# Performance work log

Measured on AMD Instinct MI355X. Metric: run time of the kernel, lower is better.

Reference implementation:

```python
import jax, jax.numpy as jnp
import numpy as np

N_NODES = 160_000
N_EDGES = 640_000
N_GRAPHS = 8_000
IN_FEATS = 74
HID = 63
MAX_DEG = 10
PRED_HID = 128
PRED_DIM = 256
BN_EPS = 1e-5
N_LAYERS = 3
PARAM_NAMES = ['W0', 'b0', 'gamma0', 'beta0', 'W1', 'b1', 'gamma1', 'beta1', 'W2', 'b2', 'gamma2', 'beta2', 'W_ng', 'b_ng', 'W_tr', 'b_tr']


def setup_inputs() -> dict:
    key = jax.random.key(0)
    ks = jax.random.split(key, 20)
    inp = {}
    inp['feats'] = jax.random.normal(ks[0], (N_NODES, IN_FEATS), dtype=jnp.float32)
    inp['src'] = jax.random.randint(ks[1], (N_EDGES,), 0, N_NODES, dtype=jnp.int32)
    inp['dst'] = jax.random.randint(ks[2], (N_EDGES,), 0, N_NODES, dtype=jnp.int32)
    # sorted graph membership: 20 nodes per graph (batched molecular graphs)
    inp['graph_ids'] = jnp.repeat(jnp.arange(N_GRAPHS, dtype=jnp.int32), N_NODES // N_GRAPHS)
    dims = [IN_FEATS, HID, HID, HID]
    for l in range(N_LAYERS):
        fi, fo = dims[l], dims[l + 1]
        inp[f'W{l}'] = jax.random.normal(ks[3 + l], (MAX_DEG, fi, fo), dtype=jnp.float32) / np.float32(np.sqrt(fi))
        inp[f'b{l}'] = jnp.zeros((MAX_DEG, fo), dtype=jnp.float32)
        inp[f'gamma{l}'] = jnp.ones((fo,), dtype=jnp.float32)
        inp[f'beta{l}'] = jnp.zeros((fo,), dtype=jnp.float32)
    inp['W_ng'] = jax.random.normal(ks[10], (HID, PRED_HID), dtype=jnp.float32) / np.float32(np.sqrt(HID))
    inp['b_ng'] = jnp.zeros((PRED_HID,), dtype=jnp.float32)
    inp['W_tr'] = jax.random.normal(ks[11], (2 * PRED_HID, PRED_DIM), dtype=jnp.float32) / np.float32(np.sqrt(2 * PRED_HID))
    inp['b_tr'] = jnp.zeros((PRED_DIM,), dtype=jnp.float32)
    return inp


def _nf_layer(h, src, dst, deg_idx, W, b, gamma, beta):
    # message passing: sum of neighbor features via copy_u / fn.sum
    neigh = jax.ops.segment_sum(h[src], dst, num_segments=N_NODES)
    tot = h + neigh  # self + neighbor sum (Duvenaud neural fingerprint)
    # degree-bucketed linear: compute all MAX_DEG transforms, select per node by degree
    z_all = jnp.einsum('ni,kio->nko', tot, W) + b  # [N, MAX_DEG, out]
    z = jnp.take_along_axis(z_all, deg_idx[:, None, None], axis=1)[:, 0, :]  # [N, out]
    z = jax.nn.relu(z)
    # batchnorm over nodes (training-mode batch statistics, eps=1e-5)
    mu = jnp.mean(z, axis=0)
    var = jnp.var(z, axis=0)
    return (z - mu) * jax.lax.rsqrt(var + BN_EPS) * gamma + beta


def _forward(feats, src, dst, graph_ids, params):
    # in-degree per node, clamped to [1, MAX_DEG] -> weight bucket index
    deg = jax.ops.segment_sum(jnp.ones((N_EDGES,), jnp.float32), dst, num_segments=N_NODES)
    deg_idx = jnp.clip(deg.astype(jnp.int32), 1, MAX_DEG) - 1
    h = feats
    for l in range(N_LAYERS):
        h = _nf_layer(h, src, dst, deg_idx, params[f'W{l}'], params[f'b{l}'],
                      params[f'gamma{l}'], params[f'beta{l}'])
    # node_to_graph linear
    h = h @ params['W_ng'] + params['b_ng']  # [N, PRED_HID]
    # SumAndMax readout over each graph
    g_sum = jax.ops.segment_sum(h, graph_ids, num_segments=N_GRAPHS)
    g_max = jax.ops.segment_max(h, graph_ids, num_segments=N_GRAPHS)
    g = jnp.tanh(jnp.concatenate([g_sum, g_max], axis=-1))  # [G, 2*PRED_HID]
    return g @ params['W_tr'] + params['b_tr']  # [G, PRED_DIM]


def reference(feats, src, dst, graph_ids, W0, b0, gamma0, beta0, W1, b1, gamma1, beta1, W2, b2, gamma2, beta2, W_ng, b_ng, W_tr, b_tr):
    params = dict(zip(PARAM_NAMES, (W0, b0, gamma0, beta0, W1, b1, gamma1, beta1, W2, b2, gamma2, beta2, W_ng, b_ng, W_tr, b_tr)))
    return _forward(feats, src, dst, graph_ids, params)
```

## Files before the change

kernel.cpp:

```cpp
#include <hip/hip_runtime.h>
#include <stdint.h>
#include <math.h>

static constexpr int NN = 160000;
static constexpr int NE = 640000;
static constexpr int NG = 8000;
static constexpr int FH  = 63;
static constexpr int ZST = 64;
static constexpr int FST = 80;
static constexpr int NB  = 128;
static constexpr int LGRID = 1536;

static constexpr size_t OFF_DEGCNT = 0;
static constexpr size_t OFF_CURSOR = 640000;
static constexpr size_t OFF_BCNT   = 1280000;
static constexpr size_t OFF_SPART  = 1280064;
static constexpr size_t ZERO_BYTES = 1673280;
static constexpr size_t OFF_ROWPTR = 1673280;
static constexpr size_t OFF_BLKSUM = 2313472;
static constexpr size_t OFF_COL    = 2315520;
static constexpr size_t OFF_BLIST  = 4875520;
static constexpr size_t OFF_AFC    = 17675520;
static constexpr size_t OFF_BNG2   = 17709312;
static constexpr size_t OFF_PBLK   = 17709824;
static constexpr size_t OFF_FB     = 17710080;
static constexpr size_t OFF_Z0     = 43310080;
static constexpr size_t OFF_Z1     = 63790080;
static constexpr size_t OFF_WNGF   = OFF_Z1;
static constexpr size_t OFF_WTRF   = OFF_Z1 + 32768;

__device__ __forceinline__ float blo(unsigned u) {
    union { unsigned i; float f; } v; v.i = u << 16; return v.f;
}
__device__ __forceinline__ float bhi(unsigned u) {
    union { unsigned i; float f; } v; v.i = u & 0xffff0000u; return v.f;
}
__device__ __forceinline__ unsigned short f2b(float f) {
    union { float f; unsigned i; } v; v.f = f;
    unsigned r = v.i + 0x7fffu + ((v.i >> 16) & 1u);
    return (unsigned short)(r >> 16);
}
__device__ __forceinline__ void acc8(float* a, uint4 q) {
    a[0] += blo(q.x); a[1] += bhi(q.x);
    a[2] += blo(q.y); a[3] += bhi(q.y);
    a[4] += blo(q.z); a[5] += bhi(q.z);
    a[6] += blo(q.w); a[7] += bhi(q.w);
}

typedef __attribute__((ext_vector_type(8))) short bf16x8;
typedef __attribute__((ext_vector_type(4))) float f32x4;
union U8 { uint4 u; bf16x8 b; };

__global__ void k_cast(const float* __restrict__ feats, unsigned short* __restrict__ fb,
                       const int* __restrict__ dst, int* __restrict__ degcnt) {
    int i = blockIdx.x * 256 + threadIdx.x;
    if (i < NE) atomicAdd(&degcnt[dst[i]], 1);
    if (i >= NN * FST) return;
    int n = i / FST, c = i - n * FST;
    float v = (c < 74) ? feats[n * 74 + c] : 0.f;
    union { float f; unsigned u; } x; x.f = v;
    unsigned r = x.u + 0x7fffu + ((x.u >> 16) & 1u);
    fb[i] = (unsigned short)(r >> 16);
}

__global__ void k_scan1(const int* __restrict__ degcnt, int* __restrict__ row_ptr,
                        int* __restrict__ blksum) {
    __shared__ int s[1024];
    int t = threadIdx.x;
    int i = blockIdx.x * 1024 + t;
    int v = (i < NN) ? degcnt[i] : 0;
    s[t] = v; __syncthreads();
    for (int off = 1; off < 1024; off <<= 1) {
        int x = (t >= off) ? s[t - off] : 0;
        __syncthreads();
        s[t] += x;
        __syncthreads();
    }
    if (i < NN) row_ptr[i + 1] = s[t];
    if (t == 1023) blksum[blockIdx.x] = s[t];
}

__global__ void k_scan2(int* __restrict__ blksum, int nblk) {
    __shared__ int s[256];
    int t = threadIdx.x;
    int v = (t < nblk) ? blksum[t] : 0;
    s[t] = v; __syncthreads();
    for (int off = 1; off < 256; off <<= 1) {
        int x = (t >= off) ? s[t - off] : 0;
        __syncthreads();
        s[t] += x;
        __syncthreads();
    }
    if (t < nblk) blksum[t] = s[t] - v;
}

__global__ void k_scan3(int* __restrict__ row_ptr, const int* __restrict__ blksum) {
    int t = threadIdx.x;
    int i = blockIdx.x * 1024 + t;
    if (i < NN) row_ptr[i + 1] += blksum[blockIdx.x];
    if (i == 0) row_ptr[0] = 0;
}

__global__ void __launch_bounds__(1024) k_bucket(
        const int* __restrict__ degcnt, const int* __restrict__ row_ptr,
        int* __restrict__ bcnt, int2* __restrict__ blist,
        int* __restrict__ pblk, int* __restrict__ ctr) {
    __shared__ int scnt[10], sbase[10];
    __shared__ int sLast;
    int tid = threadIdx.x;
    if (tid < 10) scnt[tid] = 0;
    __syncthreads();
    int n = blockIdx.x * 1024 + tid;
    int k = 0, pos = 0;
    bool v = (n < NN);
    int rp = 0;
    if (v) {
        int d = degcnt[n];
        rp = row_ptr[n];
        k = (d < 1) ? 0 : ((d > 10) ? 9 : d - 1);
        pos = atomicAdd(&scnt[k], 1);
    }
    __syncthreads();
    if (tid < 10) sbase[tid] = scnt[tid] ? atomicAdd(&bcnt[tid], scnt[tid]) : 0;
    __syncthreads();
    if (v) blist[k * NN + sbase[k] + pos] = make_int2(n, rp);

    if (tid == 0) {
        __threadfence();
        sLast = (atomicAdd(ctr, 1) == (int)gridDim.x - 1) ? 1 : 0;
    }
    __syncthreads();
    if (sLast && tid == 0) {
        __threadfence();
        const volatile int* bc = bcnt;
        int s = 0; pblk[0] = 0;
        for (int kk = 0; kk < 10; ++kk) { s += (bc[kk] + NB - 1) / NB; pblk[kk + 1] = s; }
    }
}

__global__ void k_fill(const int* __restrict__ src, const int* __restrict__ dst,
                       const int* __restrict__ row_ptr, int* __restrict__ cursor,
                       int* __restrict__ col) {
    int e = blockIdx.x * 256 + threadIdx.x;
    if (e >= NE) return;
    int d = dst[e];
    int pos = row_ptr[d] + atomicAdd(&cursor[d], 1);
    col[pos] = src[e];
}

template<int FI, int IST, bool AFF>
__global__ void __launch_bounds__(512, 4) k_layer(
    const unsigned short* __restrict__ in,
    const float* __restrict__ aff,
    const int* __restrict__ row_ptr, const int* __restrict__ col,
    const int* __restrict__ bcnt, const int2* __restrict__ blist,
    const int* __restrict__ pblk,
    const float* __restrict__ W, const float* __restrict__ B,
    unsigned short* __restrict__ zout, float* __restrict__ spart)
{
    constexpr int CH = IST / 8;
    __shared__ float sW[FI * 63 + 64];
    __shared__ float sTot[8][IST][8];
    __shared__ int   sN[8][8];
    __shared__ float sRed[2][8][64];

    int b = blockIdx.x;
    if (b >= pblk[10]) return;
    int k = 0;
#pragma unroll
    for (int i = 1; i <= 9; ++i) k += (b >= pblk[i]) ? 1 : 0;
    int base = (b - pblk[k]) * NB;
    int cnt = bcnt[k];
    if (base >= cnt) return;

    int tid = threadIdx.x;
    int wave = tid >> 6, lane = tid & 63;
    int t = lane >> 3, r = lane & 7;

    const float* Wk = W + (size_t)k * FI * 63;
#pragma unroll 4
    for (int i = tid; i < FI * 63; i += 512) sW[i] = Wk[i];
    __syncthreads();

    const uint4* inq = (const uint4*)in;
    float bterm = (lane < 63) ? B[k * 63 + lane] : 0.f;
    float lsum = 0.f, lsq = 0.f;

#pragma unroll 1
    for (int it = 0; it < NB / 64; ++it) {
        int idx = base + it * 64 + wave * 8 + t;
        if (base + it * 64 >= cnt) break;
        bool val = (idx < cnt);
        int2 bl = blist[k * NN + (val ? idx : (cnt - 1))];
        int n = bl.x, rs = bl.y;
        int dg = (k >= 1 && k <= 8) ? (k + 1) : (row_ptr[n + 1] - rs);
        if (r == 0) sN[wave][t] = val ? n : -1;

        float a[8] = {0.f, 0.f, 0.f, 0.f, 0.f, 0.f, 0.f, 0.f};

        if (k == 9) {
            {
                uint4 q = inq[(size_t)n * CH + r];
                acc8(a, q);
            }
            int d = 0;
#pragma unroll 1
            for (; d + 4 <= dg; d += 4) {
                int c0 = col[rs + d], c1 = col[rs + d + 1];
                int c2 = col[rs + d + 2], c3 = col[rs + d + 3];
                uint4 q0 = inq[(size_t)c0 * CH + r];
                uint4 q1 = inq[(size_t)c1 * CH + r];
                uint4 q2 = inq[(size_t)c2 * CH + r];
                uint4 q3 = inq[(size_t)c3 * CH + r];
                acc8(a, q0); acc8(a, q1); acc8(a, q2); acc8(a, q3);
            }
#pragma unroll 1
            for (; d < dg; ++d) {
                int c = col[rs + d];
                uint4 q = inq[(size_t)c * CH + r];
                acc8(a, q);
            }
            if constexpr (IST == 80) {
                float e2[8] = {0.f, 0.f, 0.f, 0.f, 0.f, 0.f, 0.f, 0.f};
                if (r < 2) {
                    uint4 q = inq[(size_t)n * CH + 8 + r];
                    acc8(e2, q);
                    int d2 = 0;
#pragma unroll 1
                    for (; d2 < dg; ++d2) {
                        int c = col[rs + d2];
                        uint4 p = inq[(size_t)c * CH + 8 + r];
                        acc8(e2, p);
                    }
#pragma unroll
                    for (int j = 0; j < 8; ++j) sTot[wave][64 + 8 * r + j][t] = e2[j];
                }
            }
        } else {
            if constexpr (IST == 80) {
                if (r < 2) {
                    float e2[8] = {0.f, 0.f, 0.f, 0.f, 0.f, 0.f, 0.f, 0.f};
                    uint4 ps = inq[(size_t)n * CH + 8 + r];
                    uint4 p0, p1, p2, p3, p4, p5, p6, p7, p8;
                    if (dg > 0) p0 = inq[(size_t)col[rs + 0] * CH + 8 + r];
                    if (dg > 1) p1 = inq[(size_t)col[rs + 1] * CH + 8 + r];
                    if (dg > 2) p2 = inq[(size_t)col[rs + 2] * CH + 8 + r];
                    if (dg > 3) p3 = inq[(size_t)col[rs + 3] * CH + 8 + r];
                    if (dg > 4) p4 = inq[(size_t)col[rs + 4] * CH + 8 + r];
                    if (dg > 5) p5 = inq[(size_t)col[rs + 5] * CH + 8 + r];
                    if (dg > 6) p6 = inq[(size_t)col[rs + 6] * CH + 8 + r];
                    if (dg > 7) p7 = inq[(size_t)col[rs + 7] * CH + 8 + r];
                    if (dg > 8) p8 = inq[(size_t)col[rs + 8] * CH + 8 + r];
                    acc8(e2, ps);
                    if (dg > 0) acc8(e2, p0);
                    if (dg > 1) acc8(e2, p1);
                    if (dg > 2) acc8(e2, p2);
                    if (dg > 3) acc8(e2, p3);
                    if (dg > 4) acc8(e2, p4);
                    if (dg > 5) acc8(e2, p5);
                    if (dg > 6) acc8(e2, p6);
                    if (dg > 7) acc8(e2, p7);
                    if (dg > 8) acc8(e2, p8);
#pragma unroll
                    for (int j = 0; j < 8; ++j) sTot[wave][64 + 8 * r + j][t] = e2[j];
                }
            }
            uint4 qs = inq[(size_t)n * CH + r];
            uint4 q0, q1, q2, q3, q4, q5, q6, q7, q8;
            if (dg > 0) q0 = inq[(size_t)col[rs + 0] * CH + r];
            if (dg > 1) q1 = inq[(size_t)col[rs + 1] * CH + r];
            if (dg > 2) q2 = inq[(size_t)col[rs + 2] * CH + r];
            if (dg > 3) q3 = inq[(size_t)col[rs + 3] * CH + r];
            if (dg > 4) q4 = inq[(size_t)col[rs + 4] * CH + r];
            if (dg > 5) q5 = inq[(size_t)col[rs + 5] * CH + r];
            if (dg > 6) q6 = inq[(size_t)col[rs + 6] * CH + r];
            if (dg > 7) q7 = inq[(size_t)col[rs + 7] * CH + r];
            if (dg > 8) q8 = inq[(size_t)col[rs + 8] * CH + r];
            acc8(a, qs);
            if (dg > 0) acc8(a, q0);
            if (dg > 1) acc8(a, q1);
            if (dg > 2) acc8(a, q2);
            if (dg > 3) acc8(a, q3);
            if (dg > 4) acc8(a, q4);
            if (dg > 5) acc8(a, q5);
            if (dg > 6) acc8(a, q6);
            if (dg > 7) acc8(a, q7);
            if (dg > 8) acc8(a, q8);
        }

        if constexpr (AFF) {
            const float4* af = (const float4*)aff;
            float4 A0 = af[2 * r], A1 = af[2 * r + 1];
            float4 C0 = af[16 + 2 * r], C1 = af[16 + 2 * r + 1];
            float dp1 = (float)(dg + 1);
            a[0] = A0.x * a[0] + dp1 * C0.x;  a[1] = A0.y * a[1] + dp1 * C0.y;
            a[2] = A0.z * a[2] + dp1 * C0.z;  a[3] = A0.w * a[3] + dp1 * C0.w;
            a[4] = A1.x * a[4] + dp1 * C1.x;  a[5] = A1.y * a[5] + dp1 * C1.y;
            a[6] = A1.z * a[6] + dp1 * C1.z;  a[7] = A1.w * a[7] + dp1 * C1.w;
        }

#pragma unroll
        for (int j = 0; j < 8; ++j) sTot[wave][8 * r + j][t] = a[j];

        float acc[8];
#pragma unroll
        for (int i = 0; i < 8; ++i) acc[i] = bterm;
#pragma unroll 4
        for (int j = 0; j < FI; ++j) {
            float w = sW[j * 63 + lane];
            float4 u = *(const float4*)&sTot[wave][j][0];
            float4 v = *(const float4*)&sTot[wave][j][4];
            acc[0] = fmaf(u.x, w, acc[0]); acc[1] = fmaf(u.y, w, acc[1]);
            acc[2] = fmaf(u.z, w, acc[2]); acc[3] = fmaf(u.w, w, acc[3]);
            acc[4] = fmaf(v.x, w, acc[4]); acc[5] = fmaf(v.y, w, acc[5]);
            acc[6] = fmaf(v.z, w, acc[6]); acc[7] = fmaf(v.w, w, acc[7]);
        }

#pragma unroll
        for (int tt = 0; tt < 8; ++tt) {
            int nn = sN[wave][tt];
            float z = fmaxf(acc[tt], 0.f);
            if (nn >= 0 && lane < 63) {
                zout[(size_t)nn * ZST + lane] = f2b(z);
                lsum += z; lsq += z * z;
            }
        }
    }

    sRed[0][wave][lane] = lsum;
    sRed[1][wave][lane] = lsq;
    __syncthreads();
    if (wave == 0 && lane < 63) {
        float s = 0.f, q = 0.f;
#pragma unroll
        for (int w8 = 0; w8 < 8; ++w8) {
            s += sRed[0][w8][lane];
            q += sRed[1][w8][lane];
        }
        float* sp = spart + (size_t)(blockIdx.x & 255) * 128;
        atomicAdd(&sp[lane], s);
        atomicAdd(&sp[64 + lane], q);
    }
}

__global__ void k_bn(const float* __restrict__ spart, const float* __restrict__ gamma,
                     const float* __restrict__ beta, float* __restrict__ afc) {
    __shared__ double sd[512];
    int o = blockIdx.x;
    int t = threadIdx.x;
    sd[t]       = (double)spart[t * 128 + o];
    sd[256 + t] = (double)spart[t * 128 + 64 + o];
    __syncthreads();
#pragma unroll
    for (int off = 128; off > 0; off >>= 1) {
        if (t < off) { sd[t] += sd[t + off]; sd[256 + t] += sd[256 + t + off]; }
        __syncthreads();
    }
    if (t == 0) {
        double mu  = sd[0] / NN;
        double var = sd[256] / NN - mu * mu;
        float a = (float)((double)gamma[o] / sqrt(var + 1e-5));
        float c = (float)((double)beta[o] - mu * (double)a);
        afc[o] = a;
        afc[64 + o] = c;
    }
}

__global__ void k_prepw(const float* __restrict__ W_ng, const float* __restrict__ b_ng,
                        const float* __restrict__ afc2, const float* __restrict__ W_tr,
                        unsigned short* __restrict__ WngF, unsigned short* __restrict__ WtrF,
                        float* __restrict__ bng2) {
    int bid = blockIdx.x, tid = threadIdx.x;
    if (bid == 0) {
        if (tid < 128) {
            float acc = b_ng[tid];
            for (int j = 0; j < 63; ++j)
                acc = fmaf(afc2[64 + j], W_ng[j * 128 + tid], acc);
            bng2[tid] = acc;
        }
    } else if (bid <= 64) {
        int idx = (bid - 1) * 256 + tid;
        int j = idx & 7, lane = (idx >> 3) & 63;
        int nt = (idx >> 9) & 7, kb = idx >> 12;
        int k = (kb & 1) * 32 + ((lane >> 4) << 3) + j;
        int col = nt * 16 + (lane & 15);
        float w = (k < 63) ? afc2[k] * W_ng[k * 128 + col] : 0.f;
        unsigned short hi = f2b(w);
        if (kb < 2) WngF[idx] = hi;
        else        WngF[idx] = f2b(w - blo(hi));
    } else {
        int idx = (bid - 65) * 256 + tid;
        int j = idx & 7, lane = (idx >> 3) & 63;
        int kb = (idx >> 9) & 7, nt = idx >> 12;
        int k = kb * 32 + ((lane >> 4) << 3) + j;
        int col = nt * 16 + (lane & 15);
        WtrF[idx] = f2b(W_tr[k * 256 + col]);
    }
}

__global__ void __launch_bounds__(256, 2) k_graph(
    const unsigned short* __restrict__ Z2, const unsigned short* __restrict__ WngF,
    const float* __restrict__ bng2, const unsigned short* __restrict__ WtrF,
    const float* __restrict__ b_tr, float* __restrict__ out)
{
    __shared__ unsigned short sW[16384];
    __shared__ float sT[16 * 256];
    __shared__ float sB[128];

    int tid = threadIdx.x;
    int wave = tid >> 6, lane = tid & 63;
    int gl15 = lane & 15, grp = lane >> 4;

    {
        const uint4* srcq = (const uint4*)WngF;
        uint4* dstq = (uint4*)sW;
#pragma unroll
        for (int i = 0; i < 8; ++i) dstq[tid + 256 * i] = srcq[tid + 256 * i];
    }
    if (tid < 128) sB[tid] = bng2[tid];
    __syncthreads();

    int nodeBase = blockIdx.x * 320 + wave * 80;
    const uint4* zq = (const uint4*)Z2;
    uint4 a0[5], a1[5];
#pragma unroll
    for (int m = 0; m < 5; ++m) {
        size_t row = (size_t)(nodeBase + m * 16 + gl15) * 8;
        a0[m] = zq[row + grp];
        a1[m] = zq[row + 4 + grp];
    }
    if (grp == 3) {
#pragma unroll
        for (int m = 0; m < 5; ++m) a1[m].w &= 0xffffu;
    }

    const uint4* swq = (const uint4*)sW;
    const float NEGI = -3.0e38f;

#pragma unroll 1
    for (int nt = 0; nt < 8; ++nt) {
        U8 b0, b1, b2, b3;
        b0.u = swq[(0 * 8 + nt) * 64 + lane];
        b1.u = swq[(1 * 8 + nt) * 64 + lane];
        b2.u = swq[(2 * 8 + nt) * 64 + lane];
        b3.u = swq[(3 * 8 + nt) * 64 + lane];

        f32x4 ac[5];
#pragma unroll
        for (int m = 0; m < 5; ++m) {
            U8 xa0, xa1; xa0.u = a0[m]; xa1.u = a1[m];
            f32x4 c = {0.f, 0.f, 0.f, 0.f};
            c = __builtin_amdgcn_mfma_f32_16x16x32_bf16(xa0.b, b0.b, c, 0, 0, 0);
            c = __builtin_amdgcn_mfma_f32_16x16x32_bf16(xa1.b, b1.b, c, 0, 0, 0);
            c = __builtin_amdgcn_mfma_f32_16x16x32_bf16(xa0.b, b2.b, c, 0, 0, 0);
            c = __builtin_amdgcn_mfma_f32_16x16x32_bf16(xa1.b, b3.b, c, 0, 0, 0);
            ac[m] = c;
        }

        float s[4] = {0.f, 0.f, 0.f, 0.f};
        float x[4] = {NEGI, NEGI, NEGI, NEGI};
        bool cA = lane < 16, cB = lane < 32, cC = lane < 48;
#pragma unroll
        for (int r = 0; r < 4; ++r) {
            float v0 = ac[0][r]; s[0] += v0; x[0] = fmaxf(x[0], v0);
            float v4 = ac[4][r]; s[3] += v4; x[3] = fmaxf(x[3], v4);
            float v1 = ac[1][r]; float v1a = cA ? v1 : 0.f;
            s[0] += v1a; s[1] += v1 - v1a;
            x[0] = fmaxf(x[0], cA ? v1 : NEGI); x[1] = fmaxf(x[1], cA ? NEGI : v1);
            float v2 = ac[2][r]; float v2a = cB ? v2 : 0.f;
            s[1] += v2a; s[2] += v2 - v2a;
            x[1] = fmaxf(x[1], cB ? v2 : NEGI); x[2] = fmaxf(x[2], cB ? NEGI : v2);
            float v3 = ac[3][r]; float v3a = cC ? v3 : 0.f;
            s[2] += v3a; s[3] += v3 - v3a;
            x[2] = fmaxf(x[2], cC ? v3 : NEGI); x[3] = fmaxf(x[3], cC ? NEGI : v3);
        }
#pragma unroll
        for (int g = 0; g < 4; ++g) {
            s[g] += __shfl_xor(s[g], 16);
            s[g] += __shfl_xor(s[g], 32);
            x[g] = fmaxf(x[g], __shfl_xor(x[g], 16));
            x[g] = fmaxf(x[g], __shfl_xor(x[g], 32));
        }
        if (lane < 16) {
            int c = nt * 16 + lane;
            float bb = sB[c];
#pragma unroll
            for (int g = 0; g < 4; ++g) {
                int row = wave * 4 + g;
                int swz = (row & 7) << 2;
                sT[(row * 256 + c) ^ swz]       = tanhf(s[g] + 20.f * bb);
                sT[(row * 256 + 128 + c) ^ swz] = tanhf(x[g] + bb);
            }
        }
    }
    __syncthreads();

    U8 pa[8];
    {
        int swz = (gl15 & 7) << 2;
#pragma unroll
        for (int kb = 0; kb < 8; ++kb) {
            int k8 = kb * 32 + grp * 8;
            float4 t0 = *(const float4*)&sT[(gl15 * 256 + k8) ^ swz];
            float4 t1 = *(const float4*)&sT[(gl15 * 256 + k8 + 4) ^ swz];
            unsigned u0 = (unsigned)f2b(t0.x) | ((unsigned)f2b(t0.y) << 16);
            unsigned u1 = (unsigned)f2b(t0.z) | ((unsigned)f2b(t0.w) << 16);
            unsigned u2 = (unsigned)f2b(t1.x) | ((unsigned)f2b(t1.y) << 16);
            unsigned u3 = (unsigned)f2b(t1.z) | ((unsigned)f2b(t1.w) << 16);
            pa[kb].u = make_uint4(u0, u1, u2, u3);
        }
    }
    const uint4* wtq = (const uint4*)WtrF;
    size_t gbase = (size_t)blockIdx.x * 16 * 256;
#pragma unroll 2
    for (int i = 0; i < 4; ++i) {
        int nt = wave * 4 + i;
        f32x4 c = {0.f, 0.f, 0.f, 0.f};
#pragma unroll
        for (int kb = 0; kb < 8; ++kb) {
            U8 b; b.u = wtq[(nt * 8 + kb) * 64 + lane];
            c = __builtin_amdgcn_mfma_f32_16x16x32_bf16(pa[kb].b, b.b, c, 0, 0, 0);
        }
        int d = nt * 16 + gl15;
        float btv = b_tr[d];
#pragma unroll
        for (int r = 0; r < 4; ++r) {
            int row = grp * 4 + r;
            out[gbase + (size_t)row * 256 + d] = c[r] + btv;
        }
    }
}

extern "C" void kernel_launch(void* const* d_in, const int* in_sizes, int n_in,
                              void* d_out, int out_size, void* d_ws, size_t ws_size,
                              hipStream_t stream) {
    const float* feats = (const float*)d_in[0];
    const int*   src   = (const int*)d_in[1];
    const int*   dst   = (const int*)d_in[2];
    const float* W0 = (const float*)d_in[4];
    const float* b0 = (const float*)d_in[5];
    const float* g0 = (const float*)d_in[6];
    const float* be0 = (const float*)d_in[7];
    const float* W1 = (const float*)d_in[8];
    const float* b1 = (const float*)d_in[9];
    const float* g1 = (const float*)d_in[10];
    const float* be1 = (const float*)d_in[11];
    const float* W2 = (const float*)d_in[12];
    const float* b2 = (const float*)d_in[13];
    const float* g2 = (const float*)d_in[14];
    const float* be2 = (const float*)d_in[15];
    const float* Wng = (const float*)d_in[16];
    const float* bng = (const float*)d_in[17];
    const float* Wtr = (const float*)d_in[18];
    const float* btr = (const float*)d_in[19];
    float* out = (float*)d_out;

    char* ws = (char*)d_ws;
    int*    degcnt  = (int*)(ws + OFF_DEGCNT);
    int*    cursor  = (int*)(ws + OFF_CURSOR);
    int*    bcnt    = (int*)(ws + OFF_BCNT);
    int*    ctr     = bcnt + 10;
    float*  spart   = (float*)(ws + OFF_SPART);
    int*    row_ptr = (int*)(ws + OFF_ROWPTR);
    int*    blksum  = (int*)(ws + OFF_BLKSUM);
    int*    col     = (int*)(ws + OFF_COL);
    int2*   blist   = (int2*)(ws + OFF_BLIST);
    float*  afc     = (float*)(ws + OFF_AFC);
    float*  bng2    = (float*)(ws + OFF_BNG2);
    int*    pblk    = (int*)(ws + OFF_PBLK);
    unsigned short* Fb = (unsigned short*)(ws + OFF_FB);
    unsigned short* Z0 = (unsigned short*)(ws + OFF_Z0);
    unsigned short* Z1 = (unsigned short*)(ws + OFF_Z1);
    unsigned short* Z2 = Z0;
    unsigned short* WngF = (unsigned short*)(ws + OFF_WNGF);
    unsigned short* WtrF = (unsigned short*)(ws + OFF_WTRF);

    hipMemsetAsync(d_ws, 0, ZERO_BYTES, stream);

    k_cast<<<NN * FST / 256, 256, 0, stream>>>(feats, Fb, dst, degcnt);
    k_scan1<<<157, 1024, 0, stream>>>(degcnt, row_ptr, blksum);
    k_scan2<<<1, 256, 0, stream>>>(blksum, 157);
    k_scan3<<<157, 1024, 0, stream>>>(row_ptr, blksum);
    k_bucket<<<157, 1024, 0, stream>>>(degcnt, row_ptr, bcnt, blist, pblk, ctr);
    k_fill<<<NE / 256, 256, 0, stream>>>(src, dst, row_ptr, cursor, col);

    k_layer<74, FST, false><<<LGRID, 512, 0, stream>>>(
        Fb, nullptr, row_ptr, col, bcnt, blist, pblk, W0, b0, Z0, spart);
    k_bn<<<63, 256, 0, stream>>>(spart, g0, be0, afc);
    k_layer<63, ZST, true><<<LGRID, 512, 0, stream>>>(
        Z0, afc, row_ptr, col, bcnt, blist, pblk, W1, b1, Z1, spart + 256 * 128);
    k_bn<<<63, 256, 0, stream>>>(spart + 256 * 128, g1, be1, afc + 128);
    k_layer<63, ZST, true><<<LGRID, 512, 0, stream>>>(
        Z1, afc + 128, row_ptr, col, bcnt, blist, pblk, W2, b2, Z2, spart + 2 * 256 * 128);
    k_bn<<<63, 256, 0, stream>>>(spart + 2 * 256 * 128, g2, be2, afc + 256);

    k_prepw<<<321, 256, 0, stream>>>(Wng, bng, afc + 256, Wtr, WngF, WtrF, bng2);
    k_graph<<<NG / 16, 256, 0, stream>>>(Z2, WngF, bng2, WtrF, btr, out);
}
```

Before: 500.4 us.

## Store padded per-bucket neighbor lists for aligned vector index loads

Adds a zero-initialized 12-wide neighbor table, ordered by degree-bucket slot and filled during CSR construction, for nodes with degree up to 9. The layer kernel reads all neighbor indices with three int4 loads instead of dependent scalar col[] reads. It also issues the feature gathers unconditionally so they can all be in flight together. This costs a larger zeroed workspace (about 7.7 MB more memset), extra scattered writes in k_fill, and wasted gathers of node 0 for padded slots.

```diff
diff --git a/kernel.cpp b/kernel.cpp
--- a/kernel.cpp
+++ b/kernel.cpp
@@ -15,17 +15,19 @@
 static constexpr size_t OFF_CURSOR = 640000;
 static constexpr size_t OFF_BCNT   = 1280000;
 static constexpr size_t OFF_SPART  = 1280064;
-static constexpr size_t ZERO_BYTES = 1673280;
-static constexpr size_t OFF_ROWPTR = 1673280;
-static constexpr size_t OFF_BLKSUM = 2313472;
-static constexpr size_t OFF_COL    = 2315520;
-static constexpr size_t OFF_BLIST  = 4875520;
-static constexpr size_t OFF_AFC    = 17675520;
-static constexpr size_t OFF_BNG2   = 17709312;
-static constexpr size_t OFF_PBLK   = 17709824;
-static constexpr size_t OFF_FB     = 17710080;
-static constexpr size_t OFF_Z0     = 43310080;
-static constexpr size_t OFF_Z1     = 63790080;
+static constexpr size_t OFF_NBR    = 1673280;
+static constexpr size_t ZERO_BYTES = 9353280;
+static constexpr size_t OFF_ROWPTR = 9353280;
+static constexpr size_t OFF_BLKSUM = 9994048;
+static constexpr size_t OFF_COL    = 9996096;
+static constexpr size_t OFF_NSLOT  = 12556096;
+static constexpr size_t OFF_BLIST  = 13196096;
+static constexpr size_t OFF_AFC    = 19596096;
+static constexpr size_t OFF_BNG2   = 19596864;
+static constexpr size_t OFF_PBLK   = 19597376;
+static constexpr size_t OFF_FB     = 19597504;
+static constexpr size_t OFF_Z0     = 45197504;
+static constexpr size_t OFF_Z1     = 65677504;
 static constexpr size_t OFF_WNGF   = OFF_Z1;
 static constexpr size_t OFF_WTRF   = OFF_Z1 + 32768;
 
@@ -103,7 +105,8 @@
 
 __global__ void __launch_bounds__(1024) k_bucket(
         const int* __restrict__ degcnt, const int* __restrict__ row_ptr,
-        int* __restrict__ bcnt, int2* __restrict__ blist,
+        int* __restrict__ bcnt, int* __restrict__ blist,
+        int* __restrict__ nodeslot,
         int* __restrict__ pblk, int* __restrict__ ctr) {
     __shared__ int scnt[10], sbase[10];
     __shared__ int sLast;
@@ -113,17 +116,19 @@
     int n = blockIdx.x * 1024 + tid;
     int k = 0, pos = 0;
     bool v = (n < NN);
-    int rp = 0;
     if (v) {
         int d = degcnt[n];
-        rp = row_ptr[n];
         k = (d < 1) ? 0 : ((d > 10) ? 9 : d - 1);
         pos = atomicAdd(&scnt[k], 1);
     }
     __syncthreads();
     if (tid < 10) sbase[tid] = scnt[tid] ? atomicAdd(&bcnt[tid], scnt[tid]) : 0;
     __syncthreads();
-    if (v) blist[k * NN + sbase[k] + pos] = make_int2(n, rp);
+    if (v) {
+        int slot = sbase[k] + pos;
+        blist[k * NN + slot] = n;
+        nodeslot[n] = (k << 24) | slot;
+    }
 
     if (tid == 0) {
         __threadfence();
@@ -134,18 +139,30 @@
         __threadfence();
         const volatile int* bc = bcnt;
         int s = 0; pblk[0] = 0;
-        for (int kk = 0; kk < 10; ++kk) { s += (bc[kk] + NB - 1) / NB; pblk[kk + 1] = s; }
+        int eacc = 0;
+        for (int kk = 0; kk < 10; ++kk) {
+            s += (bc[kk] + NB - 1) / NB; pblk[kk + 1] = s;
+            pblk[11 + kk] = eacc; eacc += bc[kk];
+        }
     }
 }
 
 __global__ void k_fill(const int* __restrict__ src, const int* __restrict__ dst,
                        const int* __restrict__ row_ptr, int* __restrict__ cursor,
-                       int* __restrict__ col) {
+                       int* __restrict__ col, const int* __restrict__ nodeslot,
+                       const int* __restrict__ ebase, int* __restrict__ nbr) {
     int e = blockIdx.x * 256 + threadIdx.x;
     if (e >= NE) return;
     int d = dst[e];
-    int pos = row_ptr[d] + atomicAdd(&cursor[d], 1);
-    col[pos] = src[e];
+    int sv = src[e];
+    int cur = atomicAdd(&cursor[d], 1);
+    col[row_ptr[d] + cur] = sv;
+    int s = nodeslot[d];
+    int kk = s >> 24;
+    if (kk < 9) {
+        int row = ebase[kk] + (s & 0xFFFFFF);
+        nbr[row * 12 + cur] = sv;
+    }
 }
 
 template<int FI, int IST, bool AFF>
@@ -153,8 +170,8 @@
     const unsigned short* __restrict__ in,
     const float* __restrict__ aff,
     const int* __restrict__ row_ptr, const int* __restrict__ col,
-    const int* __restrict__ bcnt, const int2* __restrict__ blist,
-    const int* __restrict__ pblk,
+    const int* __restrict__ bcnt, const int* __restrict__ blist,
+    const int* __restrict__ pblk, const int* __restrict__ nbr,
     const float* __restrict__ W, const float* __restrict__ B,
     unsigned short* __restrict__ zout, float* __restrict__ spart)
 {
@@ -172,6 +189,7 @@
     int base = (b - pblk[k]) * NB;
     int cnt = bcnt[k];
     if (base >= cnt) return;
+    int ebs = pblk[11 + k];
 
     int tid = threadIdx.x;
     int wave = tid >> 6, lane = tid & 63;
@@ -191,14 +209,17 @@
         int idx = base + it * 64 + wave * 8 + t;
         if (base + it * 64 >= cnt) break;
         bool val = (idx < cnt);
-        int2 bl = blist[k * NN + (val ? idx : (cnt - 1))];
-        int n = bl.x, rs = bl.y;
-        int dg = (k >= 1 && k <= 8) ? (k + 1) : (row_ptr[n + 1] - rs);
+        int idxc = val ? idx : (cnt - 1);
+        int n = blist[k * NN + idxc];
+        int dg;
+        if (k >= 1 && k <= 8) dg = k + 1;
+        else dg = row_ptr[n + 1] - row_ptr[n];
         if (r == 0) sN[wave][t] = val ? n : -1;
 
         float a[8] = {0.f, 0.f, 0.f, 0.f, 0.f, 0.f, 0.f, 0.f};
 
         if (k == 9) {
+            int rs = row_ptr[n];
             {
                 uint4 q = inq[(size_t)n * CH + r];
                 acc8(a, q);
@@ -237,20 +258,25 @@
                 }
             }
         } else {
+            const int4* nb4 = (const int4*)(nbr + (size_t)(ebs + idxc) * 12);
+            int4 w0 = nb4[0], w1 = nb4[1], w2 = nb4[2];
+            int c0 = w0.x, c1 = w0.y, c2 = w0.z, c3 = w0.w;
+            int c4 = w1.x, c5 = w1.y, c6 = w1.z, c7 = w1.w;
+            int c8 = w2.x;
+
             if constexpr (IST == 80) {
                 if (r < 2) {
                     float e2[8] = {0.f, 0.f, 0.f, 0.f, 0.f, 0.f, 0.f, 0.f};
                     uint4 ps = inq[(size_t)n * CH + 8 + r];
-                    uint4 p0, p1, p2, p3, p4, p5, p6, p7, p8;
-                    if (dg > 0) p0 = inq[(size_t)col[rs + 0] * CH + 8 + r];
-                    if (dg > 1) p1 = inq[(size_t)col[rs + 1] * CH + 8 + r];
-                    if (dg > 2) p2 = inq[(size_t)col[rs + 2] * CH + 8 + r];
-                    if (dg > 3) p3 = inq[(size_t)col[rs + 3] * CH + 8 + r];
-                    if (dg > 4) p4 = inq[(size_t)col[rs + 4] * CH + 8 + r];
-                    if (dg > 5) p5 = inq[(size_t)col[rs + 5] * CH + 8 + r];
-                    if (dg > 6) p6 = inq[(size_t)col[rs + 6] * CH + 8 + r];
-                    if (dg > 7) p7 = inq[(size_t)col[rs + 7] * CH + 8 + r];
-                    if (dg > 8) p8 = inq[(size_t)col[rs + 8] * CH + 8 + r];
+                    uint4 p0 = inq[(size_t)c0 * CH + 8 + r];
+                    uint4 p1 = inq[(size_t)c1 * CH + 8 + r];
+                    uint4 p2 = inq[(size_t)c2 * CH + 8 + r];
+                    uint4 p3 = inq[(size_t)c3 * CH + 8 + r];
+                    uint4 p4 = inq[(size_t)c4 * CH + 8 + r];
+                    uint4 p5 = inq[(size_t)c5 * CH + 8 + r];
+                    uint4 p6 = inq[(size_t)c6 * CH + 8 + r];
+                    uint4 p7 = inq[(size_t)c7 * CH + 8 + r];
+                    uint4 p8 = inq[(size_t)c8 * CH + 8 + r];
                     acc8(e2, ps);
                     if (dg > 0) acc8(e2, p0);
                     if (dg > 1) acc8(e2, p1);
@@ -265,17 +291,17 @@
                     for (int j = 0; j < 8; ++j) sTot[wave][64 + 8 * r + j][t] = e2[j];
                 }
             }
+
             uint4 qs = inq[(size_t)n * CH + r];
-            uint4 q0, q1, q2, q3, q4, q5, q6, q7, q8;
-            if (dg > 0) q0 = inq[(size_t)col[rs + 0] * CH + r];
-            if (dg > 1) q1 = inq[(size_t)col[rs + 1] * CH + r];
-            if (dg > 2) q2 = inq[(size_t)col[rs + 2] * CH + r];
-            if (dg > 3) q3 = inq[(size_t)col[rs + 3] * CH + r];
-            if (dg > 4) q4 = inq[(size_t)col[rs + 4] * CH + r];
-            if (dg > 5) q5 = inq[(size_t)col[rs + 5] * CH + r];
-            if (dg > 6) q6 = inq[(size_t)col[rs + 6] * CH + r];
-            if (dg > 7) q7 = inq[(size_t)col[rs + 7] * CH + r];
-            if (dg > 8) q8 = inq[(size_t)col[rs + 8] * CH + r];
+            uint4 q0 = inq[(size_t)c0 * CH + r];
+            uint4 q1 = inq[(size_t)c1 * CH + r];
+            uint4 q2 = inq[(size_t)c2 * CH + r];
+            uint4 q3 = inq[(size_t)c3 * CH + r];
+            uint4 q4 = inq[(size_t)c4 * CH + r];
+            uint4 q5 = inq[(size_t)c5 * CH + r];
+            uint4 q6 = inq[(size_t)c6 * CH + r];
+            uint4 q7 = inq[(size_t)c7 * CH + r];
+            uint4 q8 = inq[(size_t)c8 * CH + r];
             acc8(a, qs);
             if (dg > 0) acc8(a, q0);
             if (dg > 1) acc8(a, q1);
@@ -561,10 +587,12 @@
     int*    bcnt    = (int*)(ws + OFF_BCNT);
     int*    ctr     = bcnt + 10;
     float*  spart   = (float*)(ws + OFF_SPART);
+    int*    nbr     = (int*)(ws + OFF_NBR);
     int*    row_ptr = (int*)(ws + OFF_ROWPTR);
     int*    blksum  = (int*)(ws + OFF_BLKSUM);
     int*    col     = (int*)(ws + OFF_COL);
-    int2*   blist   = (int2*)(ws + OFF_BLIST);
+    int*    nslot   = (int*)(ws + OFF_NSLOT);
+    int*    blist   = (int*)(ws + OFF_BLIST);
     float*  afc     = (float*)(ws + OFF_AFC);
     float*  bng2    = (float*)(ws + OFF_BNG2);
     int*    pblk    = (int*)(ws + OFF_PBLK);
@@ -581,17 +609,17 @@
     k_scan1<<<157, 1024, 0, stream>>>(degcnt, row_ptr, blksum);
     k_scan2<<<1, 256, 0, stream>>>(blksum, 157);
     k_scan3<<<157, 1024, 0, stream>>>(row_ptr, blksum);
-    k_bucket<<<157, 1024, 0, stream>>>(degcnt, row_ptr, bcnt, blist, pblk, ctr);
-    k_fill<<<NE / 256, 256, 0, stream>>>(src, dst, row_ptr, cursor, col);
+    k_bucket<<<157, 1024, 0, stream>>>(degcnt, row_ptr, bcnt, blist, nslot, pblk, ctr);
+    k_fill<<<NE / 256, 256, 0, stream>>>(src, dst, row_ptr, cursor, col, nslot, pblk + 11, nbr);
 
     k_layer<74, FST, false><<<LGRID, 512, 0, stream>>>(
-        Fb, nullptr, row_ptr, col, bcnt, blist, pblk, W0, b0, Z0, spart);
+        Fb, nullptr, row_ptr, col, bcnt, blist, pblk, nbr, W0, b0, Z0, spart);
     k_bn<<<63, 256, 0, stream>>>(spart, g0, be0, afc);
     k_layer<63, ZST, true><<<LGRID, 512, 0, stream>>>(
-        Z0, afc, row_ptr, col, bcnt, blist, pblk, W1, b1, Z1, spart + 256 * 128);
+        Z0, afc, row_ptr, col, bcnt, blist, pblk, nbr, W1, b1, Z1, spart + 256 * 128);
     k_bn<<<63, 256, 0, stream>>>(spart + 256 * 128, g1, be1, afc + 128);
     k_layer<63, ZST, true><<<LGRID, 512, 0, stream>>>(
-        Z1, afc + 128, row_ptr, col, bcnt, blist, pblk, W2, b2, Z2, spart + 2 * 256 * 128);
+        Z1, afc + 128, row_ptr, col, bcnt, blist, pblk, nbr, W2, b2, Z2, spart + 2 * 256 * 128);
     k_bn<<<63, 256, 0, stream>>>(spart + 2 * 256 * 128, g2, be2, afc + 256);
 
     k_prepw<<<321, 256, 0, stream>>>(Wng, bng, afc + 256, Wtr, WngF, WtrF, bng2);
```

Result: faster. 428.2 us (-14.4%).
